# Optimization experiments

Hardware: AMD Instinct MI355X
Metric: run time of the kernel (lower is better)

The kernel has to match this reference:

```python
import jax, jax.numpy as jnp
import numpy as np

N_NODES = 128
N_EDGES = N_NODES * (N_NODES - 1)  # fully-connected, no self-loops
N_IN = 128
N_HID = 256
N_OUT = 128
BATCH = 32


def _build_rel_matrices():
    # one-hot incidence matrices for fully-connected off-diagonal graph
    send_idx, recv_idx = [], []
    for i in range(N_NODES):
        for j in range(N_NODES):
            if i != j:
                send_idx.append(i)
                recv_idx.append(j)
    eye = np.eye(N_NODES, dtype=np.float32)
    rel_send = eye[np.asarray(send_idx)]  # [E, N]
    rel_rec = eye[np.asarray(recv_idx)]   # [E, N]
    return jnp.asarray(rel_rec), jnp.asarray(rel_send)


def setup_inputs() -> dict:
    key = jax.random.key(0)
    k = jax.random.split(key, 6)
    rel_rec, rel_send = _build_rel_matrices()
    s1 = 1.0 / np.sqrt(2 * N_IN)
    s2 = 1.0 / np.sqrt(N_HID)
    return {
        "x": jax.random.normal(k[0], (BATCH, N_NODES, N_IN), dtype=jnp.float32),
        "rel_type": jax.random.uniform(k[1], (BATCH, N_EDGES, 4), dtype=jnp.float32),
        "rel_rec": rel_rec,
        "rel_send": rel_send,
        "W1": jax.random.normal(k[2], (2 * N_IN, N_HID), dtype=jnp.float32) * s1,
        "b1": jnp.zeros((N_HID,), dtype=jnp.float32),
        "W2": jax.random.normal(k[3], (N_HID, N_OUT), dtype=jnp.float32) * s2,
        "b2": jnp.zeros((N_OUT,), dtype=jnp.float32),
    }


def reference(x, rel_type, rel_rec, rel_send, W1, b1, W2, b2):
    # node2edge: gather sender/receiver node features via incidence matmuls
    senders = jnp.einsum('en,bnf->bef', rel_send, x)    # [B, E, n_in]
    receivers = jnp.einsum('en,bnf->bef', rel_rec, x)   # [B, E, n_in]
    edges = jnp.concatenate([senders, receivers], axis=-1)  # [B, E, 2*n_in]
    # 2-layer MLP on edges (rel_type is unused in the original forward)
    h = jax.nn.relu(edges @ W1 + b1)
    msg = h @ W2 + b2                                   # [B, E, n_out]
    # edge2node: scatter-sum then normalize by in-degree
    agg = jnp.einsum('en,bef->bnf', rel_rec, msg)       # [B, N, n_out]
    norm = rel_rec.sum(axis=0)[None, :, None]           # [1, N, 1]
    return agg / (norm + 1e-6)
```

## Files before the change

kernel.cpp:

```cpp
#include <hip/hip_runtime.h>

#define BATCH 32
#define NN    128
#define NIN   128
#define NHID  256
#define NOUT  128
#define ROWS  (BATCH * NN)

__global__ __launch_bounds__(256) void k1_sr(
    const float* __restrict__ x, const float* __restrict__ W1,
    const float* __restrict__ b1, float* __restrict__ S, float* __restrict__ R)
{
    __shared__ float xr[8][128];
    const int row0 = blockIdx.x * 8;
    const int t = threadIdx.x;
    for (int idx = t; idx < 8 * 128; idx += 256)
        xr[idx >> 7][idx & 127] = x[(size_t)row0 * NIN + idx];
    __syncthreads();

    const int c = t;
    float accs[8], accr[8];
#pragma unroll
    for (int r = 0; r < 8; ++r) { accs[r] = 0.f; accr[r] = 0.f; }

    for (int k = 0; k < NIN; k += 4) {
        float wa[4], wb[4];
#pragma unroll
        for (int kk = 0; kk < 4; ++kk) {
            wa[kk] = W1[(size_t)(k + kk) * NHID + c];
            wb[kk] = W1[(size_t)(NIN + k + kk) * NHID + c];
        }
#pragma unroll
        for (int r = 0; r < 8; ++r) {
            const float4 xv = *(const float4*)(&xr[r][k]);
            accs[r] = fmaf(xv.w, wa[3], fmaf(xv.z, wa[2], fmaf(xv.y, wa[1], fmaf(xv.x, wa[0], accs[r]))));
            accr[r] = fmaf(xv.w, wb[3], fmaf(xv.z, wb[2], fmaf(xv.y, wb[1], fmaf(xv.x, wb[0], accr[r]))));
        }
    }
    const float bias = b1[c];
#pragma unroll
    for (int r = 0; r < 8; ++r) {
        S[(size_t)(row0 + r) * NHID + c] = accs[r];
        R[(size_t)(row0 + r) * NHID + c] = accr[r] + bias;
    }
}

__global__ __launch_bounds__(256) void kB(
    const float* __restrict__ S, const float* __restrict__ R,
    const float* __restrict__ W2, const float* __restrict__ b2,
    float* __restrict__ out)
{
    __shared__ float s_lds[128][64];
    __shared__ float g_lds[8][64];
    const int blk = blockIdx.x;
    const int b   = blk >> 4;
    const int nt  = blk & 15;
    const int n0  = nt * 8;
    const int t   = threadIdx.x;
    const int cl  = t & 63;
    const int rq  = t >> 6;
    const int co  = t & 127;
    const int rh  = t >> 7;

    const float4* S4 = (const float4*)S;

    float acc[4] = {0.f, 0.f, 0.f, 0.f};

    for (int cc = 0; cc < 4; ++cc) {
        const int c0 = cc * 64;
        __syncthreads();
        for (int idx = t; idx < 2048; idx += 256) {
            const int i = idx >> 4, j = idx & 15;
            ((float4*)s_lds)[idx] = S4[(size_t)(b * NN + i) * 64 + cc * 16 + j];
        }
        float rv[2];
#pragma unroll
        for (int q = 0; q < 2; ++q)
            rv[q] = R[(size_t)(b * NN + n0 + rq * 2 + q) * NHID + c0 + cl];
        __syncthreads();

        float ag[2] = {0.f, 0.f};
        for (int i = 0; i < 128; ++i) {
            const float s = s_lds[i][cl];
            ag[0] += fmaxf(s + rv[0], 0.f);
            ag[1] += fmaxf(s + rv[1], 0.f);
        }
#pragma unroll
        for (int q = 0; q < 2; ++q) {
            const int lr = rq * 2 + q;
            ag[q] -= fmaxf(s_lds[n0 + lr][cl] + rv[q], 0.f);
            g_lds[lr][cl] = ag[q];
        }
        __syncthreads();

        for (int k = 0; k < 64; k += 2) {
            const float w0 = W2[(size_t)(c0 + k    ) * NOUT + co];
            const float w1 = W2[(size_t)(c0 + k + 1) * NOUT + co];
#pragma unroll
            for (int r = 0; r < 4; ++r) {
                acc[r] = fmaf(g_lds[rh * 4 + r][k],     w0, acc[r]);
                acc[r] = fmaf(g_lds[rh * 4 + r][k + 1], w1, acc[r]);
            }
        }
    }

    const float inv  = 1.0f / (127.0f + 1e-6f);
    const float bias = 127.0f * b2[co];
#pragma unroll
    for (int r = 0; r < 4; ++r)
        out[(size_t)(b * NN + n0 + rh * 4 + r) * NOUT + co] = (acc[r] + bias) * inv;
}

extern "C" void kernel_launch(void* const* d_in, const int* in_sizes, int n_in,
                              void* d_out, int out_size, void* d_ws, size_t ws_size,
                              hipStream_t stream)
{
    const float* x  = (const float*)d_in[0];
    const float* W1 = (const float*)d_in[4];
    const float* b1 = (const float*)d_in[5];
    const float* W2 = (const float*)d_in[6];
    const float* b2 = (const float*)d_in[7];
    float* out = (float*)d_out;

    float* S = (float*)d_ws;
    float* R = S + (size_t)ROWS * NHID;

    k1_sr<<<ROWS / 8,  256, 0, stream>>>(x, W1, b1, S, R);
    kB   <<<BATCH * 16, 256, 0, stream>>>(S, R, W2, b2, out);
}
```

Before: 127.2 us.

## Fuse both stages into one cooperative kernel with a three-phase grid-synced schedule

Merges the two kernels into one cooperative launch of 512 blocks with three phases separated by grid.sync(). The S/R projection comes first, then the relu-sum aggregation into a new global buffer G, then the W2 matmul over all 256 hidden channels in one pass. The middle phase splits work by hidden-channel chunk and node tile instead of looping over chunks inside one block, and uses float4 LDS reads. This removes the per-block serial chunk loop and a kernel launch, but adds two grid-wide barriers and an extra global round trip through G.

```diff
diff --git a/kernel.cpp b/kernel.cpp
--- a/kernel.cpp
+++ b/kernel.cpp
@@ -1,4 +1,7 @@
 #include <hip/hip_runtime.h>
+#include <hip/hip_cooperative_groups.h>
+
+namespace cg = cooperative_groups;
 
 #define BATCH 32
 #define NN    128
@@ -7,108 +10,125 @@
 #define NOUT  128
 #define ROWS  (BATCH * NN)
 
-__global__ __launch_bounds__(256) void k1_sr(
-    const float* __restrict__ x, const float* __restrict__ W1,
-    const float* __restrict__ b1, float* __restrict__ S, float* __restrict__ R)
+__global__ __launch_bounds__(256) void fused_all(
+    const float* __restrict__ x,  const float* __restrict__ W1,
+    const float* __restrict__ b1, const float* __restrict__ W2,
+    const float* __restrict__ b2, float* __restrict__ S,
+    float* __restrict__ R,        float* __restrict__ G,
+    float* __restrict__ out)
 {
-    __shared__ float xr[8][128];
-    const int row0 = blockIdx.x * 8;
-    const int t = threadIdx.x;
-    for (int idx = t; idx < 8 * 128; idx += 256)
-        xr[idx >> 7][idx & 127] = x[(size_t)row0 * NIN + idx];
-    __syncthreads();
+    cg::grid_group grid = cg::this_grid();
+    __shared__ float smem[128 * 64];
+    const int t   = threadIdx.x;
+    const int blk = blockIdx.x;
 
-    const int c = t;
-    float accs[8], accr[8];
+    {
+        float (*xr)[128] = (float (*)[128])smem;
+        const int row0 = blk * 8;
+        for (int idx = t; idx < 8 * 128; idx += 256)
+            xr[idx >> 7][idx & 127] = x[(size_t)row0 * NIN + idx];
+        __syncthreads();
+
+        const int c = t;
+        float accs[8], accr[8];
 #pragma unroll
-    for (int r = 0; r < 8; ++r) { accs[r] = 0.f; accr[r] = 0.f; }
+        for (int r = 0; r < 8; ++r) { accs[r] = 0.f; accr[r] = 0.f; }
 
-    for (int k = 0; k < NIN; k += 4) {
-        float wa[4], wb[4];
+        for (int k = 0; k < NIN; k += 4) {
+            float wa[4], wb[4];
 #pragma unroll
-        for (int kk = 0; kk < 4; ++kk) {
-            wa[kk] = W1[(size_t)(k + kk) * NHID + c];
-            wb[kk] = W1[(size_t)(NIN + k + kk) * NHID + c];
+            for (int kk = 0; kk < 4; ++kk) {
+                wa[kk] = W1[(size_t)(k + kk) * NHID + c];
+                wb[kk] = W1[(size_t)(NIN + k + kk) * NHID + c];
+            }
+#pragma unroll
+            for (int r = 0; r < 8; ++r) {
+                const float4 xv = *(const float4*)(&xr[r][k]);
+                accs[r] = fmaf(xv.w, wa[3], fmaf(xv.z, wa[2], fmaf(xv.y, wa[1], fmaf(xv.x, wa[0], accs[r]))));
+                accr[r] = fmaf(xv.w, wb[3], fmaf(xv.z, wb[2], fmaf(xv.y, wb[1], fmaf(xv.x, wb[0], accr[r]))));
+            }
         }
+        const float bias = b1[c];
 #pragma unroll
         for (int r = 0; r < 8; ++r) {
-            const float4 xv = *(const float4*)(&xr[r][k]);
-            accs[r] = fmaf(xv.w, wa[3], fmaf(xv.z, wa[2], fmaf(xv.y, wa[1], fmaf(xv.x, wa[0], accs[r]))));
-            accr[r] = fmaf(xv.w, wb[3], fmaf(xv.z, wb[2], fmaf(xv.y, wb[1], fmaf(xv.x, wb[0], accr[r]))));
+            S[(size_t)(row0 + r) * NHID + c] = accs[r];
+            R[(size_t)(row0 + r) * NHID + c] = accr[r] + bias;
         }
     }
-    const float bias = b1[c];
-#pragma unroll
-    for (int r = 0; r < 8; ++r) {
-        S[(size_t)(row0 + r) * NHID + c] = accs[r];
-        R[(size_t)(row0 + r) * NHID + c] = accr[r] + bias;
-    }
-}
+    grid.sync();
 
-__global__ __launch_bounds__(256) void kB(
-    const float* __restrict__ S, const float* __restrict__ R,
-    const float* __restrict__ W2, const float* __restrict__ b2,
-    float* __restrict__ out)
-{
-    __shared__ float s_lds[128][64];
-    __shared__ float g_lds[8][64];
-    const int blk = blockIdx.x;
-    const int b   = blk >> 4;
-    const int nt  = blk & 15;
-    const int n0  = nt * 8;
-    const int t   = threadIdx.x;
-    const int cl  = t & 63;
-    const int rq  = t >> 6;
-    const int co  = t & 127;
-    const int rh  = t >> 7;
+    {
+        const int b  = blk >> 4;
+        const int rt = (blk >> 2) & 3;
+        const int cc = blk & 3;
+        const int n0 = rt * 32;
 
-    const float4* S4 = (const float4*)S;
+        float4*       s4 = (float4*)smem;
+        const float4* S4 = (const float4*)S;
+        const float4* R4 = (const float4*)R;
+        float4*       G4 = (float4*)G;
 
-    float acc[4] = {0.f, 0.f, 0.f, 0.f};
+        for (int idx = t; idx < 2048; idx += 256)
+            s4[idx] = S4[(size_t)(b * NN + (idx >> 4)) * 64 + cc * 16 + (idx & 15)];
 
-    for (int cc = 0; cc < 4; ++cc) {
-        const int c0 = cc * 64;
-        __syncthreads();
-        for (int idx = t; idx < 2048; idx += 256) {
-            const int i = idx >> 4, j = idx & 15;
-            ((float4*)s_lds)[idx] = S4[(size_t)(b * NN + i) * 64 + cc * 16 + j];
-        }
-        float rv[2];
-#pragma unroll
-        for (int q = 0; q < 2; ++q)
-            rv[q] = R[(size_t)(b * NN + n0 + rq * 2 + q) * NHID + c0 + cl];
+        const int cg4 = t & 15;
+        const int rq  = t >> 4;
+        const int nA  = n0 + rq * 2;
+        const int nB  = nA + 1;
+        const float4 rvA = R4[(size_t)(b * NN + nA) * 64 + cc * 16 + cg4];
+        const float4 rvB = R4[(size_t)(b * NN + nB) * 64 + cc * 16 + cg4];
         __syncthreads();
 
-        float ag[2] = {0.f, 0.f};
+        float4 aA = {0.f, 0.f, 0.f, 0.f}, aB = {0.f, 0.f, 0.f, 0.f};
         for (int i = 0; i < 128; ++i) {
-            const float s = s_lds[i][cl];
-            ag[0] += fmaxf(s + rv[0], 0.f);
-            ag[1] += fmaxf(s + rv[1], 0.f);
+            const float4 s = s4[i * 16 + cg4];
+            aA.x += fmaxf(s.x + rvA.x, 0.f);  aB.x += fmaxf(s.x + rvB.x, 0.f);
+            aA.y += fmaxf(s.y + rvA.y, 0.f);  aB.y += fmaxf(s.y + rvB.y, 0.f);
+            aA.z += fmaxf(s.z + rvA.z, 0.f);  aB.z += fmaxf(s.z + rvB.z, 0.f);
+            aA.w += fmaxf(s.w + rvA.w, 0.f);  aB.w += fmaxf(s.w + rvB.w, 0.f);
         }
-#pragma unroll
-        for (int q = 0; q < 2; ++q) {
-            const int lr = rq * 2 + q;
-            ag[q] -= fmaxf(s_lds[n0 + lr][cl] + rv[q], 0.f);
-            g_lds[lr][cl] = ag[q];
-        }
+        const float4 sA = s4[nA * 16 + cg4];
+        const float4 sB = s4[nB * 16 + cg4];
+        aA.x -= fmaxf(sA.x + rvA.x, 0.f);  aB.x -= fmaxf(sB.x + rvB.x, 0.f);
+        aA.y -= fmaxf(sA.y + rvA.y, 0.f);  aB.y -= fmaxf(sB.y + rvB.y, 0.f);
+        aA.z -= fmaxf(sA.z + rvA.z, 0.f);  aB.z -= fmaxf(sB.z + rvB.z, 0.f);
+        aA.w -= fmaxf(sA.w + rvA.w, 0.f);  aB.w -= fmaxf(sB.w + rvB.w, 0.f);
+
+        G4[(size_t)(b * NN + nA) * 64 + cc * 16 + cg4] = aA;
+        G4[(size_t)(b * NN + nB) * 64 + cc * 16 + cg4] = aB;
+    }
+    grid.sync();
+
+    {
+        float (*g)[256] = (float (*)[256])smem;
+        const int row0 = blk * 8;
+        const float4* G4 = (const float4*)G;
+        float4* g4 = (float4*)smem;
+        for (int idx = t; idx < 512; idx += 256)
+            g4[idx] = G4[(size_t)row0 * 64 + idx];
         __syncthreads();
 
-        for (int k = 0; k < 64; k += 2) {
-            const float w0 = W2[(size_t)(c0 + k    ) * NOUT + co];
-            const float w1 = W2[(size_t)(c0 + k + 1) * NOUT + co];
+        const int c  = t & 127;
+        const int rh = t >> 7;
+        float acc[4] = {0.f, 0.f, 0.f, 0.f};
+
+        for (int k = 0; k < NHID; k += 4) {
+            float w[4];
+#pragma unroll
+            for (int kk = 0; kk < 4; ++kk)
+                w[kk] = W2[(size_t)(k + kk) * NOUT + c];
 #pragma unroll
             for (int r = 0; r < 4; ++r) {
-                acc[r] = fmaf(g_lds[rh * 4 + r][k],     w0, acc[r]);
-                acc[r] = fmaf(g_lds[rh * 4 + r][k + 1], w1, acc[r]);
+                const float4 gv = *(const float4*)(&g[rh * 4 + r][k]);
+                acc[r] = fmaf(gv.w, w[3], fmaf(gv.z, w[2], fmaf(gv.y, w[1], fmaf(gv.x, w[0], acc[r]))));
             }
         }
+        const float inv  = 1.0f / (127.0f + 1e-6f);
+        const float bias = 127.0f * b2[c];
+#pragma unroll
+        for (int r = 0; r < 4; ++r)
+            out[(size_t)(row0 + rh * 4 + r) * NOUT + c] = (acc[r] + bias) * inv;
     }
-
-    const float inv  = 1.0f / (127.0f + 1e-6f);
-    const float bias = 127.0f * b2[co];
-#pragma unroll
-    for (int r = 0; r < 4; ++r)
-        out[(size_t)(b * NN + n0 + rh * 4 + r) * NOUT + co] = (acc[r] + bias) * inv;
 }
 
 extern "C" void kernel_launch(void* const* d_in, const int* in_sizes, int n_in,
@@ -124,7 +144,9 @@
 
     float* S = (float*)d_ws;
     float* R = S + (size_t)ROWS * NHID;
+    float* G = R + (size_t)ROWS * NHID;
 
-    k1_sr<<<ROWS / 8,  256, 0, stream>>>(x, W1, b1, S, R);
-    kB   <<<BATCH * 16, 256, 0, stream>>>(S, R, W2, b2, out);
+    void* args[] = { (void*)&x, (void*)&W1, (void*)&b1, (void*)&W2, (void*)&b2,
+                     (void*)&S, (void*)&R, (void*)&G, (void*)&out };
+    hipLaunchCooperativeKernel((void*)fused_all, dim3(512), dim3(256), args, 0, stream);
 }
```

Result: slower. 228.4 us (+79.6%).
